# Kernel optimization log

Measured on AMD Instinct MI355X. Metric: run time of the kernel, lower is better.

Reference implementation:

```python
import jax, jax.numpy as jnp
import numpy as np

N_NODES = 100000
N_EDGES = 250000
EMB = 32
NUM_RELS2 = 100   # 2 * num_rels
NUM_TYPES = 16


def _xavier(key, shape):
    fan_in, fan_out = shape[-2], shape[-1]
    limit = float(np.sqrt(6.0 / (fan_in + fan_out)))
    return jax.random.uniform(key, shape, jnp.float32, -limit, limit)


def setup_inputs() -> dict:
    key = jax.random.key(0)
    ks = jax.random.split(key, 9)
    src_ids = jax.random.randint(ks[0], (N_NODES,), 0, N_NODES)
    edge_src = jax.random.randint(ks[1], (N_EDGES,), 0, N_NODES)
    edge_dst = jax.random.randint(ks[2], (N_EDGES,), 0, N_NODES)
    etype = jax.random.randint(ks[3], (N_EDGES,), 0, NUM_RELS2)
    entity = _xavier(ks[4], (N_NODES, EMB))
    W1 = _xavier(ks[5], (NUM_RELS2, EMB, EMB))
    W2 = _xavier(ks[6], (NUM_RELS2, EMB, NUM_TYPES))
    lambda_w = _xavier(ks[7], (NUM_TYPES, 1))
    lambda_b = jnp.zeros((1,), jnp.float32)
    return {
        "entity": entity, "W1": W1, "W2": W2,
        "lambda_w": lambda_w, "lambda_b": lambda_b,
        "src_ids": src_ids, "edge_src": edge_src,
        "edge_dst": edge_dst, "etype": etype,
    }


def _rgcn_layer(h, W, edge_src, edge_dst, etype, n_dst, activation):
    # gather per-edge relation weights [E, in, out] and per-edge bmm (as DGL does)
    msg = jnp.einsum('ed,edo->eo', h[edge_src], W[etype])  # [E, out]
    s = jax.ops.segment_sum(msg, edge_dst, num_segments=n_dst)  # [N, out]
    deg = jax.ops.segment_sum(jnp.ones((msg.shape[0],), msg.dtype),
                              edge_dst, num_segments=n_dst)
    out = s / jnp.maximum(deg, 1.0)[:, None]  # mean; 0 for isolated dst nodes
    if activation is not None:
        out = activation(out)
    return out


def reference(entity, W1, W2, lambda_w, lambda_b,
              src_ids, edge_src, edge_dst, etype):
    # eval mode: dropout disabled; self_loop=False, bias=False
    h = entity[src_ids]                                            # [N, EMB]
    h = _rgcn_layer(h, W1, edge_src, edge_dst, etype, N_NODES, jax.nn.relu)
    h = _rgcn_layer(h, W2, edge_src, edge_dst, etype, N_NODES, None)  # [N, T]
    # PonderNet loop, max_steps=2: step1 lambda from linear+sigmoid, step2 lambda=1
    lam = jax.nn.sigmoid(h @ lambda_w + lambda_b)[:, 0]            # [N]
    p = jnp.stack([lam, 1.0 - lam])                                # [2, N]
    # recomputed h at step 2 is identical (same params, no dropout)
    y = jnp.stack([h, h])                                          # [2, N, T]
    return (y, p)
```

## Files before the change

kernel.cpp:

```cpp
#include <hip/hip_runtime.h>
#include <hip/hip_bf16.h>

#define N_NODES 100000
#define N_EDGES 250000
#define EMB 32
#define TYPES 16
#define R2 100
#define SB 1024
#define NB ((N_EDGES + SB - 1) / SB)
#define CAP 4096
#define CAPD 16
#define S1 64
#define S2 64

typedef __attribute__((ext_vector_type(8))) short short8;
typedef __attribute__((ext_vector_type(4))) float f32x4;

__device__ __forceinline__ unsigned short f2bf_u(float f) {
    unsigned u = __float_as_uint(f);
    u = (u + 0x7fffu + ((u >> 16) & 1u)) >> 16;
    return (unsigned short)u;
}
__device__ __forceinline__ float bfl(unsigned u) { return __uint_as_float(u << 16); }
__device__ __forceinline__ float bfh(unsigned u) { return __uint_as_float(u & 0xffff0000u); }

__global__ __launch_bounds__(SB) void pass1_kernel(
        const int* __restrict__ etype, const int* __restrict__ edge_src,
        const int* __restrict__ edge_dst, const int* __restrict__ src_ids,
        const float* __restrict__ W1, const float* __restrict__ W2,
        int* __restrict__ rcnt, int* __restrict__ dcnt,
        unsigned short* __restrict__ pw1, unsigned short* __restrict__ pw2,
        uint2* __restrict__ epack) {
    int t = threadIdx.x, b = blockIdx.x;
    if (b < NB) {
        __shared__ int lh[R2];
        __shared__ int lbase[R2];
        if (t < R2) lh[t] = 0;
        __syncthreads();
        int e = b * SB + t;
        int r = 0, lrank = 0, pd = 0, s = 0, sid = 0;
        bool valid = e < N_EDGES;
        if (valid) {
            r = etype[e];
            lrank = atomicAdd(&lh[r], 1);
            int d = edge_dst[e];
            int drank = atomicAdd(&dcnt[d], 1);
            if (drank > CAPD - 1) drank = CAPD - 1;
            pd = (d << 4) | drank;
            s = edge_src[e];
            sid = src_ids[s];
        }
        __syncthreads();
        if (t < R2) {
            int c = lh[t];
            lbase[t] = c ? atomicAdd(&rcnt[t], c) : 0;
        }
        __syncthreads();
        if (valid) {
            uint2 v = { (unsigned)sid | (((unsigned)pd & 0x7FFFu) << 17),
                        (unsigned)s   | (((unsigned)pd >> 15) << 17) };
            epack[((size_t)r << 12) + lbase[r] + lrank] = v;
        }
    } else {
        int r = b - NB;
        const float* Wr1 = W1 + (size_t)r * (EMB * EMB);
        {
            int l = t >> 4, j = t & 15;
            int n = l & 15, q = l >> 4;
            int k = q * 8 + (j & 7);
            int col = (j < 8) ? (2 * n) : (2 * n + 1);
            pw1[(size_t)r * 1024 + t] = f2bf_u(Wr1[k * EMB + col]);
        }
        if (t < 512) {
            const float* Wr2 = W2 + (size_t)r * (EMB * TYPES);
            int l = t >> 3, j = t & 7;
            int n = l & 15, q = l >> 4;
            int k = q * 8 + j;
            pw2[(size_t)r * 512 + t] = f2bf_u(Wr2[k * TYPES + n]);
        }
    }
}

__global__ __launch_bounds__(64) void layer1_kernel(
        const float* __restrict__ entity,
        const unsigned short* __restrict__ pw1,
        const int* __restrict__ rcnt,
        const uint2* __restrict__ epack,
        unsigned int* __restrict__ msg1) {
    int r = blockIdx.x % R2, stripe = blockIdx.x / R2;
    int cnt = rcnt[r];
    int nT = (cnt + 15) >> 4;
    int lane = threadIdx.x;
    int n = lane & 15, q = lane >> 4;
    const unsigned short* pw = pw1 + (size_t)r * 1024;
    short8 b0 = *(const short8*)(pw + lane * 16);
    short8 b1 = *(const short8*)(pw + lane * 16 + 8);
    const uint2* ep = epack + ((size_t)r << 12);
    for (int g = stripe; g < nT; g += S1) {
        int base = g * 16;
        int cl = cnt - base;
        int me = n < cl ? n : cl - 1;
        uint2 E = ep[base + me];
        int sid = (int)(E.x & 0x1FFFFu);
        int pd  = (int)((E.x >> 17) | ((E.y >> 17) << 15));
        const float4* ar = (const float4*)(entity + (size_t)sid * EMB + q * 8);
        float4 v0 = ar[0], v1 = ar[1];
        short8 a;
        a[0] = (short)f2bf_u(v0.x); a[1] = (short)f2bf_u(v0.y);
        a[2] = (short)f2bf_u(v0.z); a[3] = (short)f2bf_u(v0.w);
        a[4] = (short)f2bf_u(v1.x); a[5] = (short)f2bf_u(v1.y);
        a[6] = (short)f2bf_u(v1.z); a[7] = (short)f2bf_u(v1.w);
        f32x4 c0 = {0.f,0.f,0.f,0.f}, c1 = {0.f,0.f,0.f,0.f};
        c0 = __builtin_amdgcn_mfma_f32_16x16x32_bf16(a, b0, c0, 0, 0, 0);
        c1 = __builtin_amdgcn_mfma_f32_16x16x32_bf16(a, b1, c1, 0, 0, 0);
#pragma unroll
        for (int i = 0; i < 4; ++i) {
            int row = q * 4 + i;
            int p = __shfl(pd, row);
            if (row < cl) {
                unsigned w = (unsigned)f2bf_u(c0[i]) | ((unsigned)f2bf_u(c1[i]) << 16);
                msg1[(size_t)p * 16 + n] = w;
            }
        }
    }
}

__global__ void reduce1_kernel(const unsigned int* __restrict__ msg1,
                               const int* __restrict__ dcnt,
                               unsigned int* __restrict__ h1bf) {
    int t = blockIdx.x * blockDim.x + threadIdx.x;
    if (t >= N_NODES * 16) return;
    int nn = t >> 4, cp = t & 15;
    int cnt = dcnt[nn];
    int km = cnt < CAPD ? cnt : CAPD;
    int s = nn << 4;
    float sx = 0.f, sy = 0.f;
    for (int k = 0; k < km; ++k) {
        unsigned v = msg1[(size_t)(s + k) * 16 + cp];
        sx += bfl(v); sy += bfh(v);
    }
    float inv = 1.0f / fmaxf((float)cnt, 1.0f);
    unsigned lo = f2bf_u(fmaxf(sx * inv, 0.f));
    unsigned hi = f2bf_u(fmaxf(sy * inv, 0.f));
    h1bf[t] = lo | (hi << 16);
}

__global__ __launch_bounds__(64) void layer2_kernel(
        const unsigned short* __restrict__ h1bf,
        const unsigned short* __restrict__ pw2,
        const int* __restrict__ rcnt,
        const uint2* __restrict__ epack,
        unsigned int* __restrict__ msg2) {
    int r = blockIdx.x % R2, stripe = blockIdx.x / R2;
    int cnt = rcnt[r];
    int nT = (cnt + 15) >> 4;
    int lane = threadIdx.x;
    int n = lane & 15, q = lane >> 4;
    short8 b = *(const short8*)(pw2 + (size_t)r * 512 + lane * 8);
    const uint2* ep = epack + ((size_t)r << 12);
    for (int g = stripe; g < nT; g += S2) {
        int base = g * 16;
        int cl = cnt - base;
        int me = n < cl ? n : cl - 1;
        uint2 E = ep[base + me];
        int s  = (int)(E.y & 0x1FFFFu);
        int pd = (int)((E.x >> 17) | ((E.y >> 17) << 15));
        short8 a = *(const short8*)(h1bf + (size_t)s * EMB + q * 8);
        f32x4 c = {0.f,0.f,0.f,0.f};
        c = __builtin_amdgcn_mfma_f32_16x16x32_bf16(a, b, c, 0, 0, 0);
#pragma unroll
        for (int i = 0; i < 4; ++i) {
            int row = q * 4 + i;
            int p = __shfl(pd, row);
            unsigned myb = (unsigned)f2bf_u(c[i]);
            unsigned ob  = (unsigned)__shfl_xor((int)myb, 1);
            if (row < cl && !(n & 1)) {
                msg2[(size_t)p * 8 + (n >> 1)] = myb | (ob << 16);
            }
        }
    }
}

__global__ void reduce2_head_kernel(const unsigned int* __restrict__ msg2,
                                    const int* __restrict__ dcnt,
                                    const float* __restrict__ lw,
                                    const float* __restrict__ lb,
                                    float* __restrict__ out) {
    int nn = blockIdx.x * blockDim.x + threadIdx.x;
    if (nn >= N_NODES) return;
    int cnt = dcnt[nn];
    int km = cnt < CAPD ? cnt : CAPD;
    int s = nn << 4;
    float h[TYPES];
#pragma unroll
    for (int j = 0; j < TYPES; ++j) h[j] = 0.f;
    for (int k = 0; k < km; ++k) {
        const uint4* row = (const uint4*)(msg2 + (size_t)(s + k) * 8);
        uint4 A = row[0], B = row[1];
        h[0] += bfl(A.x);  h[1] += bfh(A.x);  h[2] += bfl(A.y);  h[3] += bfh(A.y);
        h[4] += bfl(A.z);  h[5] += bfh(A.z);  h[6] += bfl(A.w);  h[7] += bfh(A.w);
        h[8] += bfl(B.x);  h[9] += bfh(B.x);  h[10] += bfl(B.y); h[11] += bfh(B.y);
        h[12] += bfl(B.z); h[13] += bfh(B.z); h[14] += bfl(B.w); h[15] += bfh(B.w);
    }
    float inv = 1.0f / fmaxf((float)cnt, 1.0f);
    float dot = 0.f;
#pragma unroll
    for (int j = 0; j < TYPES; ++j) { h[j] *= inv; dot += h[j] * lw[j]; }
    dot += lb[0];
    float lam = 1.0f / (1.0f + expf(-dot));

    float4* y0 = (float4*)(out + (size_t)nn * TYPES);
    float4* y1 = (float4*)(out + (size_t)N_NODES * TYPES + (size_t)nn * TYPES);
#pragma unroll
    for (int j = 0; j < 4; ++j) {
        float4 v = { h[4*j], h[4*j+1], h[4*j+2], h[4*j+3] };
        y0[j] = v; y1[j] = v;
    }
    out[(size_t)2 * N_NODES * TYPES + nn] = lam;
    out[(size_t)2 * N_NODES * TYPES + N_NODES + nn] = 1.0f - lam;
}

extern "C" void kernel_launch(void* const* d_in, const int* in_sizes, int n_in,
                              void* d_out, int out_size, void* d_ws, size_t ws_size,
                              hipStream_t stream) {
    const float* entity = (const float*)d_in[0];
    const float* W1     = (const float*)d_in[1];
    const float* W2     = (const float*)d_in[2];
    const float* lw     = (const float*)d_in[3];
    const float* lb     = (const float*)d_in[4];
    const int* src_ids  = (const int*)d_in[5];
    const int* edge_src = (const int*)d_in[6];
    const int* edge_dst = (const int*)d_in[7];
    const int* etype    = (const int*)d_in[8];
    float* out = (float*)d_out;

    unsigned int* W = (unsigned int*)d_ws;
    int* dcnt   = (int*)(W + 0);
    int* rcnt   = (int*)(W + 100000);
    uint2* epack = (uint2*)(W + 100128);
    unsigned short* pw1 = (unsigned short*)(W + 919328);
    unsigned short* pw2 = (unsigned short*)(W + 970528);
    unsigned int* h1bf  = W + 996128;
    unsigned int* msg1  = W + 2596128;
    unsigned int* msg2  = W + 28196128;

    (void)hipMemsetAsync(d_ws, 0, 100128 * sizeof(int), stream);

    pass1_kernel<<<NB + R2, SB, 0, stream>>>(etype, edge_src, edge_dst, src_ids,
                                             W1, W2, rcnt, dcnt, pw1, pw2, epack);
    layer1_kernel<<<R2 * S1, 64, 0, stream>>>(entity, pw1, rcnt, epack, msg1);
    reduce1_kernel<<<(N_NODES * 16 + 255) / 256, 256, 0, stream>>>(msg1, dcnt, h1bf);
    layer2_kernel<<<R2 * S2, 64, 0, stream>>>((const unsigned short*)h1bf, pw2,
                                              rcnt, epack, msg2);
    reduce2_head_kernel<<<(N_NODES + 255) / 256, 256, 0, stream>>>(
        msg2, dcnt, lw, lb, out);
}
```

Before: 131.1 us.

## Replace per-destination message slots with float atomic accumulation

Per-edge messages are no longer written as bf16 into fixed 16-slot buckets per destination and summed afterwards. Both layers now add their results directly into fp32 per-node accumulators with relaxed device-scope atomics, and the reduce kernels become a simple scale (plus ReLU or the head). The accumulator region is zeroed inside pass1, and the dcnt rank tracking is dropped. This removes the large sparse msg buffers and the strided reduction reads, and it lifts the 16-edge cap that could drop messages for high in-degree nodes. In exchange it adds atomic traffic and makes the summation order nondeterministic.

```diff
diff --git a/kernel.cpp b/kernel.cpp
--- a/kernel.cpp
+++ b/kernel.cpp
@@ -9,7 +9,6 @@
 #define SB 1024
 #define NB ((N_EDGES + SB - 1) / SB)
 #define CAP 4096
-#define CAPD 16
 #define S1 64
 #define S2 64
 
@@ -21,8 +20,12 @@
     u = (u + 0x7fffu + ((u >> 16) & 1u)) >> 16;
     return (unsigned short)u;
 }
-__device__ __forceinline__ float bfl(unsigned u) { return __uint_as_float(u << 16); }
-__device__ __forceinline__ float bfh(unsigned u) { return __uint_as_float(u & 0xffff0000u); }
+__device__ __forceinline__ void atomF(float* p, float v) {
+    __hip_atomic_fetch_add(p, v, __ATOMIC_RELAXED, __HIP_MEMORY_SCOPE_AGENT);
+}
+
+#define ZBASE 2596128u
+#define ZN4   1200000u
 
 __global__ __launch_bounds__(SB) void pass1_kernel(
         const int* __restrict__ etype, const int* __restrict__ edge_src,
@@ -30,23 +33,26 @@
         const float* __restrict__ W1, const float* __restrict__ W2,
         int* __restrict__ rcnt, int* __restrict__ dcnt,
         unsigned short* __restrict__ pw1, unsigned short* __restrict__ pw2,
-        uint2* __restrict__ epack) {
+        uint2* __restrict__ epack, uint4* __restrict__ zbase) {
     int t = threadIdx.x, b = blockIdx.x;
+    {
+        uint4 z = {0u, 0u, 0u, 0u};
+        for (unsigned i = b * SB + t; i < ZN4; i += (NB + R2) * SB)
+            zbase[i] = z;
+    }
     if (b < NB) {
         __shared__ int lh[R2];
         __shared__ int lbase[R2];
         if (t < R2) lh[t] = 0;
         __syncthreads();
         int e = b * SB + t;
-        int r = 0, lrank = 0, pd = 0, s = 0, sid = 0;
+        int r = 0, lrank = 0, d = 0, s = 0, sid = 0;
         bool valid = e < N_EDGES;
         if (valid) {
             r = etype[e];
             lrank = atomicAdd(&lh[r], 1);
-            int d = edge_dst[e];
-            int drank = atomicAdd(&dcnt[d], 1);
-            if (drank > CAPD - 1) drank = CAPD - 1;
-            pd = (d << 4) | drank;
+            d = edge_dst[e];
+            atomicAdd(&dcnt[d], 1);
             s = edge_src[e];
             sid = src_ids[s];
         }
@@ -57,8 +63,8 @@
         }
         __syncthreads();
         if (valid) {
-            uint2 v = { (unsigned)sid | (((unsigned)pd & 0x7FFFu) << 17),
-                        (unsigned)s   | (((unsigned)pd >> 15) << 17) };
+            uint2 v = { (unsigned)sid | (((unsigned)d & 0x7FFFu) << 17),
+                        (unsigned)s   | (((unsigned)d >> 15) << 17) };
             epack[((size_t)r << 12) + lbase[r] + lrank] = v;
         }
     } else {
@@ -86,7 +92,7 @@
         const unsigned short* __restrict__ pw1,
         const int* __restrict__ rcnt,
         const uint2* __restrict__ epack,
-        unsigned int* __restrict__ msg1) {
+        float* __restrict__ h1acc) {
     int r = blockIdx.x % R2, stripe = blockIdx.x / R2;
     int cnt = rcnt[r];
     int nT = (cnt + 15) >> 4;
@@ -102,7 +108,7 @@
         int me = n < cl ? n : cl - 1;
         uint2 E = ep[base + me];
         int sid = (int)(E.x & 0x1FFFFu);
-        int pd  = (int)((E.x >> 17) | ((E.y >> 17) << 15));
+        int d   = (int)((E.x >> 17) | ((E.y >> 17) << 15));
         const float4* ar = (const float4*)(entity + (size_t)sid * EMB + q * 8);
         float4 v0 = ar[0], v1 = ar[1];
         short8 a;
@@ -116,32 +122,26 @@
 #pragma unroll
         for (int i = 0; i < 4; ++i) {
             int row = q * 4 + i;
-            int p = __shfl(pd, row);
+            int dd = __shfl(d, row);
             if (row < cl) {
-                unsigned w = (unsigned)f2bf_u(c0[i]) | ((unsigned)f2bf_u(c1[i]) << 16);
-                msg1[(size_t)p * 16 + n] = w;
+                float* hp = h1acc + (size_t)dd * EMB + 2 * n;
+                atomF(hp,     c0[i]);
+                atomF(hp + 1, c1[i]);
             }
         }
     }
 }
 
-__global__ void reduce1_kernel(const unsigned int* __restrict__ msg1,
+__global__ void reduce1_kernel(const float* __restrict__ h1acc,
                                const int* __restrict__ dcnt,
                                unsigned int* __restrict__ h1bf) {
     int t = blockIdx.x * blockDim.x + threadIdx.x;
     if (t >= N_NODES * 16) return;
-    int nn = t >> 4, cp = t & 15;
-    int cnt = dcnt[nn];
-    int km = cnt < CAPD ? cnt : CAPD;
-    int s = nn << 4;
-    float sx = 0.f, sy = 0.f;
-    for (int k = 0; k < km; ++k) {
-        unsigned v = msg1[(size_t)(s + k) * 16 + cp];
-        sx += bfl(v); sy += bfh(v);
-    }
-    float inv = 1.0f / fmaxf((float)cnt, 1.0f);
-    unsigned lo = f2bf_u(fmaxf(sx * inv, 0.f));
-    unsigned hi = f2bf_u(fmaxf(sy * inv, 0.f));
+    int nn = t >> 4;
+    float2 v = ((const float2*)h1acc)[t];
+    float inv = 1.0f / fmaxf((float)dcnt[nn], 1.0f);
+    unsigned lo = f2bf_u(fmaxf(v.x * inv, 0.f));
+    unsigned hi = f2bf_u(fmaxf(v.y * inv, 0.f));
     h1bf[t] = lo | (hi << 16);
 }
 
@@ -150,7 +150,7 @@
         const unsigned short* __restrict__ pw2,
         const int* __restrict__ rcnt,
         const uint2* __restrict__ epack,
-        unsigned int* __restrict__ msg2) {
+        float* __restrict__ h2acc) {
     int r = blockIdx.x % R2, stripe = blockIdx.x / R2;
     int cnt = rcnt[r];
     int nT = (cnt + 15) >> 4;
@@ -163,49 +163,40 @@
         int cl = cnt - base;
         int me = n < cl ? n : cl - 1;
         uint2 E = ep[base + me];
-        int s  = (int)(E.y & 0x1FFFFu);
-        int pd = (int)((E.x >> 17) | ((E.y >> 17) << 15));
+        int s = (int)(E.y & 0x1FFFFu);
+        int d = (int)((E.x >> 17) | ((E.y >> 17) << 15));
         short8 a = *(const short8*)(h1bf + (size_t)s * EMB + q * 8);
         f32x4 c = {0.f,0.f,0.f,0.f};
         c = __builtin_amdgcn_mfma_f32_16x16x32_bf16(a, b, c, 0, 0, 0);
 #pragma unroll
         for (int i = 0; i < 4; ++i) {
             int row = q * 4 + i;
-            int p = __shfl(pd, row);
-            unsigned myb = (unsigned)f2bf_u(c[i]);
-            unsigned ob  = (unsigned)__shfl_xor((int)myb, 1);
-            if (row < cl && !(n & 1)) {
-                msg2[(size_t)p * 8 + (n >> 1)] = myb | (ob << 16);
-            }
-        }
-    }
-}
-
-__global__ void reduce2_head_kernel(const unsigned int* __restrict__ msg2,
+            int dd = __shfl(d, row);
+            if (row < cl)
+                atomF(h2acc + (size_t)dd * TYPES + n, c[i]);
+        }
+    }
+}
+
+__global__ void reduce2_head_kernel(const float* __restrict__ h2acc,
                                     const int* __restrict__ dcnt,
                                     const float* __restrict__ lw,
                                     const float* __restrict__ lb,
                                     float* __restrict__ out) {
     int nn = blockIdx.x * blockDim.x + threadIdx.x;
     if (nn >= N_NODES) return;
-    int cnt = dcnt[nn];
-    int km = cnt < CAPD ? cnt : CAPD;
-    int s = nn << 4;
+    const float4* hr = (const float4*)(h2acc + (size_t)nn * TYPES);
+    float4 H[4] = { hr[0], hr[1], hr[2], hr[3] };
+    float inv = 1.0f / fmaxf((float)dcnt[nn], 1.0f);
     float h[TYPES];
 #pragma unroll
-    for (int j = 0; j < TYPES; ++j) h[j] = 0.f;
-    for (int k = 0; k < km; ++k) {
-        const uint4* row = (const uint4*)(msg2 + (size_t)(s + k) * 8);
-        uint4 A = row[0], B = row[1];
-        h[0] += bfl(A.x);  h[1] += bfh(A.x);  h[2] += bfl(A.y);  h[3] += bfh(A.y);
-        h[4] += bfl(A.z);  h[5] += bfh(A.z);  h[6] += bfl(A.w);  h[7] += bfh(A.w);
-        h[8] += bfl(B.x);  h[9] += bfh(B.x);  h[10] += bfl(B.y); h[11] += bfh(B.y);
-        h[12] += bfl(B.z); h[13] += bfh(B.z); h[14] += bfl(B.w); h[15] += bfh(B.w);
-    }
-    float inv = 1.0f / fmaxf((float)cnt, 1.0f);
+    for (int j = 0; j < 4; ++j) {
+        h[4*j]   = H[j].x * inv; h[4*j+1] = H[j].y * inv;
+        h[4*j+2] = H[j].z * inv; h[4*j+3] = H[j].w * inv;
+    }
     float dot = 0.f;
 #pragma unroll
-    for (int j = 0; j < TYPES; ++j) { h[j] *= inv; dot += h[j] * lw[j]; }
+    for (int j = 0; j < TYPES; ++j) dot += h[j] * lw[j];
     dot += lb[0];
     float lam = 1.0f / (1.0f + expf(-dot));
 
@@ -241,17 +232,19 @@
     unsigned short* pw1 = (unsigned short*)(W + 919328);
     unsigned short* pw2 = (unsigned short*)(W + 970528);
     unsigned int* h1bf  = W + 996128;
-    unsigned int* msg1  = W + 2596128;
-    unsigned int* msg2  = W + 28196128;
+    float* h1acc = (float*)(W + ZBASE);
+    float* h2acc = (float*)(W + 5796128);
 
     (void)hipMemsetAsync(d_ws, 0, 100128 * sizeof(int), stream);
 
     pass1_kernel<<<NB + R2, SB, 0, stream>>>(etype, edge_src, edge_dst, src_ids,
-                                             W1, W2, rcnt, dcnt, pw1, pw2, epack);
-    layer1_kernel<<<R2 * S1, 64, 0, stream>>>(entity, pw1, rcnt, epack, msg1);
-    reduce1_kernel<<<(N_NODES * 16 + 255) / 256, 256, 0, stream>>>(msg1, dcnt, h1bf);
+                                             W1, W2, rcnt, dcnt, pw1, pw2, epack,
+                                             (uint4*)(W + ZBASE));
+    layer1_kernel<<<R2 * S1, 64, 0, stream>>>(entity, pw1, rcnt, epack, h1acc);
+    reduce1_kernel<<<(N_NODES * 16 + 255) / 256, 256, 0, stream>>>(
+        h1acc, dcnt, h1bf);
     layer2_kernel<<<R2 * S2, 64, 0, stream>>>((const unsigned short*)h1bf, pw2,
-                                              rcnt, epack, msg2);
+                                              rcnt, epack, h2acc);
     reduce2_head_kernel<<<(N_NODES + 255) / 256, 256, 0, stream>>>(
-        msg2, dcnt, lw, lb, out);
-}
+        h2acc, dcnt, lw, lb, out);
+}
```

New measurement: 177.0 us. 1.35x slower.

## Fuse per-edge transforms with destination reduction using dst-bucketed edge lists

Applied to the files above, without the earlier changes.

Edges are now bucketed by destination node instead of by relation type. Each node's message computation and mean reduction happen in one kernel per layer, using scalar FMAs and shuffles instead of MFMA. This removes the msg1/msg2 intermediate buffers and two reduce kernels, saving a lot of global memory traffic. In exchange it gives up matrix-core use and does scattered per-edge weight reads across relations, which makes the inner loop more ALU-heavy and divergent.

```diff
diff --git a/kernel.cpp b/kernel.cpp
--- a/kernel.cpp
+++ b/kernel.cpp
@@ -8,13 +8,9 @@
 #define R2 100
 #define SB 1024
 #define NB ((N_EDGES + SB - 1) / SB)
-#define CAP 4096
 #define CAPD 16
-#define S1 64
-#define S2 64
 
 typedef __attribute__((ext_vector_type(8))) short short8;
-typedef __attribute__((ext_vector_type(4))) float f32x4;
 
 __device__ __forceinline__ unsigned short f2bf_u(float f) {
     unsigned u = __float_as_uint(f);
@@ -28,196 +24,131 @@
         const int* __restrict__ etype, const int* __restrict__ edge_src,
         const int* __restrict__ edge_dst, const int* __restrict__ src_ids,
         const float* __restrict__ W1, const float* __restrict__ W2,
-        int* __restrict__ rcnt, int* __restrict__ dcnt,
-        unsigned short* __restrict__ pw1, unsigned short* __restrict__ pw2,
-        uint2* __restrict__ epack) {
+        int* __restrict__ dcnt,
+        unsigned* __restrict__ pwc1, unsigned* __restrict__ pwc2,
+        uint2* __restrict__ epackD) {
     int t = threadIdx.x, b = blockIdx.x;
     if (b < NB) {
-        __shared__ int lh[R2];
-        __shared__ int lbase[R2];
-        if (t < R2) lh[t] = 0;
-        __syncthreads();
         int e = b * SB + t;
-        int r = 0, lrank = 0, pd = 0, s = 0, sid = 0;
-        bool valid = e < N_EDGES;
-        if (valid) {
-            r = etype[e];
-            lrank = atomicAdd(&lh[r], 1);
+        if (e < N_EDGES) {
+            int r = etype[e];
             int d = edge_dst[e];
-            int drank = atomicAdd(&dcnt[d], 1);
-            if (drank > CAPD - 1) drank = CAPD - 1;
-            pd = (d << 4) | drank;
-            s = edge_src[e];
-            sid = src_ids[s];
-        }
-        __syncthreads();
-        if (t < R2) {
-            int c = lh[t];
-            lbase[t] = c ? atomicAdd(&rcnt[t], c) : 0;
-        }
-        __syncthreads();
-        if (valid) {
-            uint2 v = { (unsigned)sid | (((unsigned)pd & 0x7FFFu) << 17),
-                        (unsigned)s   | (((unsigned)pd >> 15) << 17) };
-            epack[((size_t)r << 12) + lbase[r] + lrank] = v;
+            int k = atomicAdd(&dcnt[d], 1);
+            if (k > CAPD - 1) k = CAPD - 1;
+            int s = edge_src[e];
+            int sid = src_ids[s];
+            uint2 v = { (unsigned)sid | ((unsigned)r << 17),
+                        (unsigned)s   | ((unsigned)r << 17) };
+            epackD[(d << 4) | k] = v;
         }
     } else {
         int r = b - NB;
-        const float* Wr1 = W1 + (size_t)r * (EMB * EMB);
-        {
-            int l = t >> 4, j = t & 15;
-            int n = l & 15, q = l >> 4;
-            int k = q * 8 + (j & 7);
-            int col = (j < 8) ? (2 * n) : (2 * n + 1);
-            pw1[(size_t)r * 1024 + t] = f2bf_u(Wr1[k * EMB + col]);
-        }
         if (t < 512) {
+            int m = t >> 4, c = t & 15;
+            const float* Wr1 = W1 + (size_t)r * (EMB * EMB);
+            unsigned lo = f2bf_u(Wr1[m * EMB + 2 * c]);
+            unsigned hi = f2bf_u(Wr1[m * EMB + 2 * c + 1]);
+            pwc1[(size_t)r * 512 + t] = lo | (hi << 16);
+        } else if (t < 768) {
+            int idx = t - 512;
+            int m = idx >> 3, c = idx & 7;
             const float* Wr2 = W2 + (size_t)r * (EMB * TYPES);
-            int l = t >> 3, j = t & 7;
-            int n = l & 15, q = l >> 4;
-            int k = q * 8 + j;
-            pw2[(size_t)r * 512 + t] = f2bf_u(Wr2[k * TYPES + n]);
+            unsigned lo = f2bf_u(Wr2[m * TYPES + 2 * c]);
+            unsigned hi = f2bf_u(Wr2[m * TYPES + 2 * c + 1]);
+            pwc2[(size_t)r * 256 + idx] = lo | (hi << 16);
         }
     }
 }
 
-__global__ __launch_bounds__(64) void layer1_kernel(
+__global__ __launch_bounds__(256) void fused1_kernel(
         const float* __restrict__ entity,
-        const unsigned short* __restrict__ pw1,
-        const int* __restrict__ rcnt,
-        const uint2* __restrict__ epack,
-        unsigned int* __restrict__ msg1) {
-    int r = blockIdx.x % R2, stripe = blockIdx.x / R2;
-    int cnt = rcnt[r];
-    int nT = (cnt + 15) >> 4;
-    int lane = threadIdx.x;
-    int n = lane & 15, q = lane >> 4;
-    const unsigned short* pw = pw1 + (size_t)r * 1024;
-    short8 b0 = *(const short8*)(pw + lane * 16);
-    short8 b1 = *(const short8*)(pw + lane * 16 + 8);
-    const uint2* ep = epack + ((size_t)r << 12);
-    for (int g = stripe; g < nT; g += S1) {
-        int base = g * 16;
-        int cl = cnt - base;
-        int me = n < cl ? n : cl - 1;
-        uint2 E = ep[base + me];
-        int sid = (int)(E.x & 0x1FFFFu);
-        int pd  = (int)((E.x >> 17) | ((E.y >> 17) << 15));
-        const float4* ar = (const float4*)(entity + (size_t)sid * EMB + q * 8);
-        float4 v0 = ar[0], v1 = ar[1];
-        short8 a;
-        a[0] = (short)f2bf_u(v0.x); a[1] = (short)f2bf_u(v0.y);
-        a[2] = (short)f2bf_u(v0.z); a[3] = (short)f2bf_u(v0.w);
-        a[4] = (short)f2bf_u(v1.x); a[5] = (short)f2bf_u(v1.y);
-        a[6] = (short)f2bf_u(v1.z); a[7] = (short)f2bf_u(v1.w);
-        f32x4 c0 = {0.f,0.f,0.f,0.f}, c1 = {0.f,0.f,0.f,0.f};
-        c0 = __builtin_amdgcn_mfma_f32_16x16x32_bf16(a, b0, c0, 0, 0, 0);
-        c1 = __builtin_amdgcn_mfma_f32_16x16x32_bf16(a, b1, c1, 0, 0, 0);
+        const unsigned* __restrict__ pwc1,
+        const int* __restrict__ dcnt,
+        const uint2* __restrict__ epackD,
+        unsigned* __restrict__ h1bf) {
+    int tid = blockIdx.x * 256 + threadIdx.x;
+    int nn = tid >> 4;
+    if (nn >= N_NODES) return;
+    int lane = threadIdx.x & 63;
+    int base = lane & 48;
+    int c = lane & 15;
+    int cnt = dcnt[nn];
+    int km = cnt < CAPD ? cnt : CAPD;
+    uint2 E = epackD[(nn << 4) + c];
+    float d0 = 0.f, d1 = 0.f;
+    for (int k = 0; k < km; ++k) {
+        unsigned ei = (unsigned)__shfl((int)E.x, base + k);
+        int sid = (int)(ei & 0x1FFFFu);
+        int r   = (int)(ei >> 17);
+        const float* row = entity + (size_t)sid * EMB;
+        float e0 = row[c];
+        float e1 = row[c + 16];
+        const unsigned* wb = pwc1 + (size_t)r * 512;
 #pragma unroll
-        for (int i = 0; i < 4; ++i) {
-            int row = q * 4 + i;
-            int p = __shfl(pd, row);
-            if (row < cl) {
-                unsigned w = (unsigned)f2bf_u(c0[i]) | ((unsigned)f2bf_u(c1[i]) << 16);
-                msg1[(size_t)p * 16 + n] = w;
-            }
+        for (int m = 0; m < 32; ++m) {
+            float a = __shfl(m < 16 ? e0 : e1, base + (m & 15));
+            unsigned w = wb[m * 16 + c];
+            d0 += a * bfl(w);
+            d1 += a * bfh(w);
         }
     }
+    float inv = 1.0f / fmaxf((float)cnt, 1.0f);
+    unsigned lo = f2bf_u(fmaxf(d0 * inv, 0.f));
+    unsigned hi = f2bf_u(fmaxf(d1 * inv, 0.f));
+    h1bf[(nn << 4) + c] = lo | (hi << 16);
 }
 
-__global__ void reduce1_kernel(const unsigned int* __restrict__ msg1,
-                               const int* __restrict__ dcnt,
-                               unsigned int* __restrict__ h1bf) {
-    int t = blockIdx.x * blockDim.x + threadIdx.x;
-    if (t >= N_NODES * 16) return;
-    int nn = t >> 4, cp = t & 15;
+__global__ __launch_bounds__(256) void fused2_kernel(
+        const unsigned* __restrict__ h1bf,
+        const unsigned* __restrict__ pwc2,
+        const int* __restrict__ dcnt,
+        const uint2* __restrict__ epackD,
+        const float* __restrict__ lw, const float* __restrict__ lb,
+        float* __restrict__ out) {
+    int tid = blockIdx.x * 256 + threadIdx.x;
+    int nn = tid >> 3;
+    if (nn >= N_NODES) return;
+    int lane = threadIdx.x & 63;
+    int base = lane & 56;
+    int c = lane & 7;
     int cnt = dcnt[nn];
     int km = cnt < CAPD ? cnt : CAPD;
-    int s = nn << 4;
-    float sx = 0.f, sy = 0.f;
+    uint2 Ea = epackD[(nn << 4) + c];
+    uint2 Eb = epackD[(nn << 4) + 8 + c];
+    float d0 = 0.f, d1 = 0.f;
     for (int k = 0; k < km; ++k) {
-        unsigned v = msg1[(size_t)(s + k) * 16 + cp];
-        sx += bfl(v); sy += bfh(v);
+        int sel = (k < 8) ? (int)Ea.y : (int)Eb.y;
+        unsigned ei = (unsigned)__shfl(sel, base + (k & 7));
+        int s = (int)(ei & 0x1FFFFu);
+        int r = (int)(ei >> 17);
+        unsigned H0 = h1bf[(size_t)s * 16 + c];
+        unsigned H1 = h1bf[(size_t)s * 16 + 8 + c];
+        const unsigned* wb = pwc2 + (size_t)r * 256;
+#pragma unroll
+        for (int p = 0; p < 16; ++p) {
+            unsigned hw = (unsigned)__shfl(p < 8 ? (int)H0 : (int)H1, base + (p & 7));
+            float a0 = bfl(hw), a1 = bfh(hw);
+            unsigned w0 = wb[(2 * p) * 8 + c];
+            unsigned w1 = wb[(2 * p + 1) * 8 + c];
+            d0 += a0 * bfl(w0); d1 += a0 * bfh(w0);
+            d0 += a1 * bfl(w1); d1 += a1 * bfh(w1);
+        }
     }
     float inv = 1.0f / fmaxf((float)cnt, 1.0f);
-    unsigned lo = f2bf_u(fmaxf(sx * inv, 0.f));
-    unsigned hi = f2bf_u(fmaxf(sy * inv, 0.f));
-    h1bf[t] = lo | (hi << 16);
-}
+    float h0 = d0 * inv, h1v = d1 * inv;
+    float part = h0 * lw[2 * c] + h1v * lw[2 * c + 1];
+    part += __shfl_xor(part, 1);
+    part += __shfl_xor(part, 2);
+    part += __shfl_xor(part, 4);
+    float lam = 1.0f / (1.0f + expf(-(part + lb[0])));
 
-__global__ __launch_bounds__(64) void layer2_kernel(
-        const unsigned short* __restrict__ h1bf,
-        const unsigned short* __restrict__ pw2,
-        const int* __restrict__ rcnt,
-        const uint2* __restrict__ epack,
-        unsigned int* __restrict__ msg2) {
-    int r = blockIdx.x % R2, stripe = blockIdx.x / R2;
-    int cnt = rcnt[r];
-    int nT = (cnt + 15) >> 4;
-    int lane = threadIdx.x;
-    int n = lane & 15, q = lane >> 4;
-    short8 b = *(const short8*)(pw2 + (size_t)r * 512 + lane * 8);
-    const uint2* ep = epack + ((size_t)r << 12);
-    for (int g = stripe; g < nT; g += S2) {
-        int base = g * 16;
-        int cl = cnt - base;
-        int me = n < cl ? n : cl - 1;
-        uint2 E = ep[base + me];
-        int s  = (int)(E.y & 0x1FFFFu);
-        int pd = (int)((E.x >> 17) | ((E.y >> 17) << 15));
-        short8 a = *(const short8*)(h1bf + (size_t)s * EMB + q * 8);
-        f32x4 c = {0.f,0.f,0.f,0.f};
-        c = __builtin_amdgcn_mfma_f32_16x16x32_bf16(a, b, c, 0, 0, 0);
-#pragma unroll
-        for (int i = 0; i < 4; ++i) {
-            int row = q * 4 + i;
-            int p = __shfl(pd, row);
-            unsigned myb = (unsigned)f2bf_u(c[i]);
-            unsigned ob  = (unsigned)__shfl_xor((int)myb, 1);
-            if (row < cl && !(n & 1)) {
-                msg2[(size_t)p * 8 + (n >> 1)] = myb | (ob << 16);
-            }
-        }
+    float2 hv = { h0, h1v };
+    ((float2*)(out + (size_t)nn * TYPES))[c] = hv;
+    ((float2*)(out + (size_t)N_NODES * TYPES + (size_t)nn * TYPES))[c] = hv;
+    if (c == 0) {
+        out[(size_t)2 * N_NODES * TYPES + nn] = lam;
+        out[(size_t)2 * N_NODES * TYPES + N_NODES + nn] = 1.0f - lam;
     }
-}
-
-__global__ void reduce2_head_kernel(const unsigned int* __restrict__ msg2,
-                                    const int* __restrict__ dcnt,
-                                    const float* __restrict__ lw,
-                                    const float* __restrict__ lb,
-                                    float* __restrict__ out) {
-    int nn = blockIdx.x * blockDim.x + threadIdx.x;
-    if (nn >= N_NODES) return;
-    int cnt = dcnt[nn];
-    int km = cnt < CAPD ? cnt : CAPD;
-    int s = nn << 4;
-    float h[TYPES];
-#pragma unroll
-    for (int j = 0; j < TYPES; ++j) h[j] = 0.f;
-    for (int k = 0; k < km; ++k) {
-        const uint4* row = (const uint4*)(msg2 + (size_t)(s + k) * 8);
-        uint4 A = row[0], B = row[1];
-        h[0] += bfl(A.x);  h[1] += bfh(A.x);  h[2] += bfl(A.y);  h[3] += bfh(A.y);
-        h[4] += bfl(A.z);  h[5] += bfh(A.z);  h[6] += bfl(A.w);  h[7] += bfh(A.w);
-        h[8] += bfl(B.x);  h[9] += bfh(B.x);  h[10] += bfl(B.y); h[11] += bfh(B.y);
-        h[12] += bfl(B.z); h[13] += bfh(B.z); h[14] += bfl(B.w); h[15] += bfh(B.w);
-    }
-    float inv = 1.0f / fmaxf((float)cnt, 1.0f);
-    float dot = 0.f;
-#pragma unroll
-    for (int j = 0; j < TYPES; ++j) { h[j] *= inv; dot += h[j] * lw[j]; }
-    dot += lb[0];
-    float lam = 1.0f / (1.0f + expf(-dot));
-
-    float4* y0 = (float4*)(out + (size_t)nn * TYPES);
-    float4* y1 = (float4*)(out + (size_t)N_NODES * TYPES + (size_t)nn * TYPES);
-#pragma unroll
-    for (int j = 0; j < 4; ++j) {
-        float4 v = { h[4*j], h[4*j+1], h[4*j+2], h[4*j+3] };
-        y0[j] = v; y1[j] = v;
-    }
-    out[(size_t)2 * N_NODES * TYPES + nn] = lam;
-    out[(size_t)2 * N_NODES * TYPES + N_NODES + nn] = 1.0f - lam;
 }
 
 extern "C" void kernel_launch(void* const* d_in, const int* in_sizes, int n_in,
@@ -235,23 +166,18 @@
     float* out = (float*)d_out;
 
     unsigned int* W = (unsigned int*)d_ws;
-    int* dcnt   = (int*)(W + 0);
-    int* rcnt   = (int*)(W + 100000);
-    uint2* epack = (uint2*)(W + 100128);
-    unsigned short* pw1 = (unsigned short*)(W + 919328);
-    unsigned short* pw2 = (unsigned short*)(W + 970528);
-    unsigned int* h1bf  = W + 996128;
-    unsigned int* msg1  = W + 2596128;
-    unsigned int* msg2  = W + 28196128;
+    int* dcnt       = (int*)(W + 0);
+    uint2* epackD   = (uint2*)(W + 100000);
+    unsigned* pwc1  = W + 3300000;
+    unsigned* pwc2  = W + 3351200;
+    unsigned* h1bf  = W + 3376800;
 
-    (void)hipMemsetAsync(d_ws, 0, 100128 * sizeof(int), stream);
+    (void)hipMemsetAsync(d_ws, 0, 100000 * sizeof(int), stream);
 
     pass1_kernel<<<NB + R2, SB, 0, stream>>>(etype, edge_src, edge_dst, src_ids,
-                                             W1, W2, rcnt, dcnt, pw1, pw2, epack);
-    layer1_kernel<<<R2 * S1, 64, 0, stream>>>(entity, pw1, rcnt, epack, msg1);
-    reduce1_kernel<<<(N_NODES * 16 + 255) / 256, 256, 0, stream>>>(msg1, dcnt, h1bf);
-    layer2_kernel<<<R2 * S2, 64, 0, stream>>>((const unsigned short*)h1bf, pw2,
-                                              rcnt, epack, msg2);
-    reduce2_head_kernel<<<(N_NODES + 255) / 256, 256, 0, stream>>>(
-        msg2, dcnt, lw, lb, out);
+                                             W1, W2, dcnt, pwc1, pwc2, epackD);
+    fused1_kernel<<<(N_NODES * 16) / 256, 256, 0, stream>>>(
+        entity, pwc1, dcnt, epackD, h1bf);
+    fused2_kernel<<<(N_NODES * 8) / 256, 256, 0, stream>>>(
+        h1bf, pwc2, dcnt, epackD, lw, lb, out);
 }
```

After: 169.6 us. 29.3% more time.
